# Kernel tuning notes

Hardware: AMD Instinct MI355X
Metric: run time of the kernel (lower is better)

## Reference

```python
import jax, jax.numpy as jnp
import numpy as np

B, T, N_EMBD, HEAD = 8, 2048, 1024, 64


def setup_inputs() -> dict:
    key = jax.random.key(0)
    kx, kq, kk, kv = jax.random.split(key, 4)
    s = 1.0 / np.sqrt(N_EMBD)
    return {
        "x": jax.random.normal(kx, (B, T, N_EMBD), dtype=jnp.float32),
        "Wq": jax.random.normal(kq, (N_EMBD, HEAD), dtype=jnp.float32) * s,
        "Wk": jax.random.normal(kk, (N_EMBD, HEAD), dtype=jnp.float32) * s,
        "Wv": jax.random.normal(kv, (N_EMBD, HEAD), dtype=jnp.float32) * s,
    }


def reference(x, Wq, Wk, Wv):
    # x: [B, T, C] with C = n_embd
    Bs, Ts, C = x.shape
    q = jnp.einsum('btc,ch->bth', x, Wq)  # [B,T,H]
    k = jnp.einsum('btc,ch->bth', x, Wk)
    v = jnp.einsum('btc,ch->bth', x, Wv)
    # NOTE: original scales by C**-0.5 where C = n_embd (input dim), not head_size
    scale = jnp.asarray(C, x.dtype) ** -0.5
    wei = jnp.einsum('bth,bsh->bts', q, k) * scale  # [B,T,T]
    causal = jnp.tril(jnp.ones((Ts, Ts), dtype=bool))
    wei = jnp.where(causal, wei, jnp.asarray(-jnp.inf, wei.dtype))
    wei = jax.nn.softmax(wei, axis=-1)
    out = jnp.einsum('bts,bsh->bth', wei, v)  # [B,T,H]
    return out
```

## Files before the change

kernel.cpp:

```cpp
#include <hip/hip_runtime.h>
#include <hip/hip_bf16.h>
#include <math.h>

#define B_ 8
#define T_ 2048
#define C_ 1024
#define H_ 64

typedef __attribute__((ext_vector_type(8))) __bf16 bf16x8;
typedef __attribute__((ext_vector_type(4))) float f32x4;

static __device__ inline unsigned short f2bf_u(float f) {
    __bf16 b = (__bf16)f;
    return __builtin_bit_cast(unsigned short, b);
}
static __device__ inline unsigned int pack2(float lo, float hi) {
    return (unsigned int)f2bf_u(lo) | ((unsigned int)f2bf_u(hi) << 16);
}

__global__ void prep_w_kernel(const float* __restrict__ Wq,
                              const float* __restrict__ Wk,
                              const float* __restrict__ Wv,
                              unsigned short* __restrict__ Wp) {
    int idx = blockIdx.x * 256 + threadIdx.x;
    if (idx >= C_ * 192) return;
    int k = idx / 192;
    int n = idx % 192;
    const float* W = (n < 64) ? Wq : (n < 128) ? Wk : Wv;
    float val = W[k * 64 + (n & 63)];
    Wp[((size_t)(k >> 5) * 192 + n) * 32 + (k & 31)] = f2bf_u(val);
}

#define XPAD 40
__global__ __launch_bounds__(256, 4) void proj_kernel(
        const float* __restrict__ x, const unsigned short* __restrict__ Wp,
        unsigned short* __restrict__ q, unsigned short* __restrict__ k,
        unsigned short* __restrict__ vT) {
    __shared__ unsigned short xbf[3][16][XPAD];
    const int wave = threadIdx.x >> 6;
    const int lane = threadIdx.x & 63;
    const int col  = lane & 15;
    const int quad = lane >> 4;
    const int row0 = blockIdx.x * 16;
    const int n0   = wave * 48;

    const int srow = lane >> 2;
    const int scol = (lane & 3) * 8;
    const float* sbase = x + (size_t)(row0 + srow) * C_ + scol;

    f32x4 acc[3];
    #pragma unroll
    for (int i = 0; i < 3; i++) acc[i] = (f32x4){0.f, 0.f, 0.f, 0.f};

    if (wave < 2) {
        const float4* p = (const float4*)(sbase + wave * 32);
        float4 u0 = p[0], u1 = p[1];
        bf16x8 w;
        w[0] = (__bf16)u0.x; w[1] = (__bf16)u0.y; w[2] = (__bf16)u0.z; w[3] = (__bf16)u0.w;
        w[4] = (__bf16)u1.x; w[5] = (__bf16)u1.y; w[6] = (__bf16)u1.z; w[7] = (__bf16)u1.w;
        *(bf16x8*)&xbf[wave][srow][scol] = w;
    }
    const unsigned short* wb = Wp + (size_t)(n0 + col) * 32 + quad * 8;
    bf16x8 bcur0 = *(const bf16x8*)(wb);
    bf16x8 bcur1 = *(const bf16x8*)(wb + 16 * 32);
    bf16x8 bcur2 = *(const bf16x8*)(wb + 32 * 32);
    __syncthreads();

    #pragma unroll 2
    for (int kt = 0; kt < 32; kt++) {
        const bool own = (kt + 2 < 32) && (((kt + 2) & 3) == wave);
        float4 u0, u1;
        if (own) {
            const float4* p = (const float4*)(sbase + (kt + 2) * 32);
            u0 = p[0]; u1 = p[1];
        }
        bf16x8 bn0, bn1, bn2;
        if (kt + 1 < 32) {
            const unsigned short* wn = wb + (size_t)(kt + 1) * 192 * 32;
            bn0 = *(const bf16x8*)(wn);
            bn1 = *(const bf16x8*)(wn + 16 * 32);
            bn2 = *(const bf16x8*)(wn + 32 * 32);
        }
        bf16x8 a = *(const bf16x8*)&xbf[kt % 3][col][quad * 8];
        acc[0] = __builtin_amdgcn_mfma_f32_16x16x32_bf16(a, bcur0, acc[0], 0, 0, 0);
        acc[1] = __builtin_amdgcn_mfma_f32_16x16x32_bf16(a, bcur1, acc[1], 0, 0, 0);
        acc[2] = __builtin_amdgcn_mfma_f32_16x16x32_bf16(a, bcur2, acc[2], 0, 0, 0);
        bcur0 = bn0; bcur1 = bn1; bcur2 = bn2;
        if (own) {
            bf16x8 w;
            w[0] = (__bf16)u0.x; w[1] = (__bf16)u0.y; w[2] = (__bf16)u0.z; w[3] = (__bf16)u0.w;
            w[4] = (__bf16)u1.x; w[5] = (__bf16)u1.y; w[6] = (__bf16)u1.z; w[7] = (__bf16)u1.w;
            *(bf16x8*)&xbf[(kt + 2) % 3][srow][scol] = w;
        }
        __syncthreads();
    }

    #pragma unroll
    for (int nt = 0; nt < 3; nt++) {
        f32x4 s = acc[nt];
        int c = n0 + nt * 16;
        int g = c >> 6;
        if (g < 2) {
            unsigned short* dst = (g == 0) ? q : k;
            int cc = (c & 63) + col;
            int grow = row0 + quad * 4;
            #pragma unroll
            for (int r = 0; r < 4; r++)
                dst[(size_t)(grow + r) * 64 + cc] = f2bf_u(s[r]);
        } else {
            int hh = (c - 128) + col;
            int bi = row0 >> 11, trow = (row0 & 2047) + quad * 4;
            ushort4 pk;
            pk.x = f2bf_u(s[0]); pk.y = f2bf_u(s[1]);
            pk.z = f2bf_u(s[2]); pk.w = f2bf_u(s[3]);
            *(ushort4*)(vT + ((size_t)bi * 64 + hh) * T_ + trow) = pk;
        }
    }
}

__global__ __launch_bounds__(256, 4) void attn_kernel(
        const unsigned short* __restrict__ q, const unsigned short* __restrict__ k,
        const unsigned short* __restrict__ vT, float* __restrict__ out) {
    __shared__ unsigned int tbuf[4][2][16 * 20];
    __shared__ float so[4][16][68];
    __shared__ float sl[4][16];
    const int wave = threadIdx.x >> 6;
    const int lane = threadIdx.x & 63;
    const int col  = lane & 15;
    const int quad = lane >> 4;
    const int bi = blockIdx.x & 7;
    const int ti = 127 - (blockIdx.x >> 3);
    const int t0 = ti * 16;
    const unsigned short* qb = q  + (size_t)bi * T_ * 64;
    const unsigned short* kb = k  + (size_t)bi * T_ * 64;
    const unsigned short* vb = vT + (size_t)bi * 64 * T_;

    bf16x8 qf0 = *(const bf16x8*)(qb + (size_t)(t0 + col) * 64 + quad * 8);
    bf16x8 qf1 = *(const bf16x8*)(qb + (size_t)(t0 + col) * 64 + 32 + quad * 8);

    f32x4 o[4];
    #pragma unroll
    for (int i = 0; i < 4; i++) o[i] = (f32x4){0.f, 0.f, 0.f, 0.f};
    float lacc = 0.f;
    const float cs = 0.03125f * 1.44269504088896f;
    const int qrow = t0 + col;

    const int nit = (t0 + 47) >> 5;
    const int ci  = (nit + 3) >> 2;
    const int it0 = wave * ci;
    const int it1 = min(it0 + ci, nit);

    for (int it = it0; it < it1; ++it) {
        const int s0 = it * 32;
        bf16x8 kf00 = *(const bf16x8*)(kb + (size_t)(s0 + col) * 64 + quad * 8);
        bf16x8 kf01 = *(const bf16x8*)(kb + (size_t)(s0 + col) * 64 + 32 + quad * 8);
        bf16x8 kf10 = *(const bf16x8*)(kb + (size_t)(s0 + 16 + col) * 64 + quad * 8);
        bf16x8 kf11 = *(const bf16x8*)(kb + (size_t)(s0 + 16 + col) * 64 + 32 + quad * 8);
        f32x4 sa = (f32x4){0.f, 0.f, 0.f, 0.f};
        f32x4 sb = (f32x4){0.f, 0.f, 0.f, 0.f};
        sa = __builtin_amdgcn_mfma_f32_16x16x32_bf16(kf00, qf0, sa, 0, 0, 0);
        sa = __builtin_amdgcn_mfma_f32_16x16x32_bf16(kf01, qf1, sa, 0, 0, 0);
        sb = __builtin_amdgcn_mfma_f32_16x16x32_bf16(kf10, qf0, sb, 0, 0, 0);
        sb = __builtin_amdgcn_mfma_f32_16x16x32_bf16(kf11, qf1, sb, 0, 0, 0);

        float pa[4], pb[4];
        #pragma unroll
        for (int r = 0; r < 4; r++) {
            int ka = s0 + quad * 4 + r;
            pa[r] = (ka      <= qrow) ? exp2f(sa[r] * cs) : 0.f;
            pb[r] = (ka + 16 <= qrow) ? exp2f(sb[r] * cs) : 0.f;
            lacc += pa[r] + pb[r];
        }
        unsigned int* tb = &tbuf[wave][it & 1][0];
        *(uint2*)&tb[col * 20 + 2 * quad] =
            make_uint2(pack2(pa[0], pa[1]), pack2(pa[2], pa[3]));
        *(uint2*)&tb[col * 20 + 8 + 2 * quad] =
            make_uint2(pack2(pb[0], pb[1]), pack2(pb[2], pb[3]));
        bf16x8 pf = *(const bf16x8*)&tb[col * 20 + 4 * quad];
        #pragma unroll
        for (int ht = 0; ht < 4; ht++) {
            bf16x8 vf = *(const bf16x8*)(vb + (size_t)(ht * 16 + col) * T_ + s0 + quad * 8);
            o[ht] = __builtin_amdgcn_mfma_f32_16x16x32_bf16(vf, pf, o[ht], 0, 0, 0);
        }
    }

    lacc += __shfl_xor(lacc, 16);
    lacc += __shfl_xor(lacc, 32);
    if (quad == 0) sl[wave][col] = lacc;
    #pragma unroll
    for (int ht = 0; ht < 4; ht++)
        *(f32x4*)&so[wave][col][ht * 16 + quad * 4] = o[ht];
    __syncthreads();

    for (int e = threadIdx.x; e < 1024; e += 256) {
        int qq = e >> 6, h = e & 63;
        float L = sl[0][qq] + sl[1][qq] + sl[2][qq] + sl[3][qq];
        float val = so[0][qq][h] + so[1][qq][h] + so[2][qq][h] + so[3][qq][h];
        out[((size_t)bi * T_ + t0 + qq) * 64 + h] = val / L;
    }
}

extern "C" void kernel_launch(void* const* d_in, const int* in_sizes, int n_in,
                              void* d_out, int out_size, void* d_ws, size_t ws_size,
                              hipStream_t stream) {
    const float* x  = (const float*)d_in[0];
    const float* Wq = (const float*)d_in[1];
    const float* Wk = (const float*)d_in[2];
    const float* Wv = (const float*)d_in[3];
    float* out = (float*)d_out;

    unsigned short* Wp  = (unsigned short*)d_ws;
    unsigned short* qws = (unsigned short*)((char*)d_ws + 0x60000);
    unsigned short* kws = (unsigned short*)((char*)d_ws + 0x60000 + 0x200000);
    unsigned short* vws = (unsigned short*)((char*)d_ws + 0x60000 + 0x400000);

    prep_w_kernel<<<(C_ * 192 + 255) / 256, 256, 0, stream>>>(Wq, Wk, Wv, Wp);
    proj_kernel<<<(B_ * T_) / 16, 256, 0, stream>>>(x, Wp, qws, kws, vws);
    attn_kernel<<<(B_ * T_) / 16, 256, 0, stream>>>(qws, kws, vws, out);
}
```

Measured before the change: 161.9 us.

## Stage x in larger double-buffered chunks and split attention keys over eight waves

The projection kernel now has all threads load and convert 256-column chunks of x into a double-buffered shared tile. It syncs once per 8 k-steps instead of every step, prefetching two chunks ahead in registers. The attention kernel moves to 512 threads with eight waves sharing the key range, so each query tile's causal loop is shorter. This costs more shared memory and registers per block, plus a larger final reduction across waves.

```diff
diff --git a/kernel.cpp b/kernel.cpp
--- a/kernel.cpp
+++ b/kernel.cpp
@@ -16,6 +16,12 @@
 }
 static __device__ inline unsigned int pack2(float lo, float hi) {
     return (unsigned int)f2bf_u(lo) | ((unsigned int)f2bf_u(hi) << 16);
+}
+static __device__ inline bf16x8 cvt8(float4 a, float4 b) {
+    bf16x8 w;
+    w[0] = (__bf16)a.x; w[1] = (__bf16)a.y; w[2] = (__bf16)a.z; w[3] = (__bf16)a.w;
+    w[4] = (__bf16)b.x; w[5] = (__bf16)b.y; w[6] = (__bf16)b.z; w[7] = (__bf16)b.w;
+    return w;
 }
 
 __global__ void prep_w_kernel(const float* __restrict__ Wq,
@@ -31,12 +37,12 @@
     Wp[((size_t)(k >> 5) * 192 + n) * 32 + (k & 31)] = f2bf_u(val);
 }
 
-#define XPAD 40
+#define XSTR 264
 __global__ __launch_bounds__(256, 4) void proj_kernel(
         const float* __restrict__ x, const unsigned short* __restrict__ Wp,
         unsigned short* __restrict__ q, unsigned short* __restrict__ k,
         unsigned short* __restrict__ vT) {
-    __shared__ unsigned short xbf[3][16][XPAD];
+    __shared__ unsigned short xb[2][16][XSTR];
     const int wave = threadIdx.x >> 6;
     const int lane = threadIdx.x & 63;
     const int col  = lane & 15;
@@ -44,53 +50,57 @@
     const int row0 = blockIdx.x * 16;
     const int n0   = wave * 48;
 
-    const int srow = lane >> 2;
-    const int scol = (lane & 3) * 8;
-    const float* sbase = x + (size_t)(row0 + srow) * C_ + scol;
+    const int srow = threadIdx.x >> 4;
+    const int sf   = (threadIdx.x & 15) * 16;
+    const float* sb = x + (size_t)(row0 + srow) * C_ + sf;
 
     f32x4 acc[3];
     #pragma unroll
     for (int i = 0; i < 3; i++) acc[i] = (f32x4){0.f, 0.f, 0.f, 0.f};
 
-    if (wave < 2) {
-        const float4* p = (const float4*)(sbase + wave * 32);
-        float4 u0 = p[0], u1 = p[1];
-        bf16x8 w;
-        w[0] = (__bf16)u0.x; w[1] = (__bf16)u0.y; w[2] = (__bf16)u0.z; w[3] = (__bf16)u0.w;
-        w[4] = (__bf16)u1.x; w[5] = (__bf16)u1.y; w[6] = (__bf16)u1.z; w[7] = (__bf16)u1.w;
-        *(bf16x8*)&xbf[wave][srow][scol] = w;
-    }
+    {
+        float4 t0 = *(const float4*)(sb + 0),  t1 = *(const float4*)(sb + 4);
+        float4 t2 = *(const float4*)(sb + 8),  t3 = *(const float4*)(sb + 12);
+        *(bf16x8*)&xb[0][srow][sf]     = cvt8(t0, t1);
+        *(bf16x8*)&xb[0][srow][sf + 8] = cvt8(t2, t3);
+    }
+    float4 l0 = *(const float4*)(sb + 256), l1 = *(const float4*)(sb + 260);
+    float4 l2 = *(const float4*)(sb + 264), l3 = *(const float4*)(sb + 268);
+
     const unsigned short* wb = Wp + (size_t)(n0 + col) * 32 + quad * 8;
     bf16x8 bcur0 = *(const bf16x8*)(wb);
     bf16x8 bcur1 = *(const bf16x8*)(wb + 16 * 32);
     bf16x8 bcur2 = *(const bf16x8*)(wb + 32 * 32);
     __syncthreads();
 
-    #pragma unroll 2
-    for (int kt = 0; kt < 32; kt++) {
-        const bool own = (kt + 2 < 32) && (((kt + 2) & 3) == wave);
-        float4 u0, u1;
-        if (own) {
-            const float4* p = (const float4*)(sbase + (kt + 2) * 32);
-            u0 = p[0]; u1 = p[1];
-        }
-        bf16x8 bn0, bn1, bn2;
-        if (kt + 1 < 32) {
-            const unsigned short* wn = wb + (size_t)(kt + 1) * 192 * 32;
-            bn0 = *(const bf16x8*)(wn);
-            bn1 = *(const bf16x8*)(wn + 16 * 32);
-            bn2 = *(const bf16x8*)(wn + 32 * 32);
-        }
-        bf16x8 a = *(const bf16x8*)&xbf[kt % 3][col][quad * 8];
-        acc[0] = __builtin_amdgcn_mfma_f32_16x16x32_bf16(a, bcur0, acc[0], 0, 0, 0);
-        acc[1] = __builtin_amdgcn_mfma_f32_16x16x32_bf16(a, bcur1, acc[1], 0, 0, 0);
-        acc[2] = __builtin_amdgcn_mfma_f32_16x16x32_bf16(a, bcur2, acc[2], 0, 0, 0);
-        bcur0 = bn0; bcur1 = bn1; bcur2 = bn2;
-        if (own) {
-            bf16x8 w;
-            w[0] = (__bf16)u0.x; w[1] = (__bf16)u0.y; w[2] = (__bf16)u0.z; w[3] = (__bf16)u0.w;
-            w[4] = (__bf16)u1.x; w[5] = (__bf16)u1.y; w[6] = (__bf16)u1.z; w[7] = (__bf16)u1.w;
-            *(bf16x8*)&xbf[(kt + 2) % 3][srow][scol] = w;
+    for (int p = 0; p < 4; ++p) {
+        float4 f0, f1, f2, f3;
+        if (p + 2 < 4) {
+            const float* s2 = sb + (p + 2) * 256;
+            f0 = *(const float4*)(s2 + 0);  f1 = *(const float4*)(s2 + 4);
+            f2 = *(const float4*)(s2 + 8);  f3 = *(const float4*)(s2 + 12);
+        }
+        #pragma unroll
+        for (int kt = 0; kt < 8; ++kt) {
+            const int ktg = p * 8 + kt;
+            bf16x8 bn0, bn1, bn2;
+            if (ktg + 1 < 32) {
+                const unsigned short* wn = wb + (size_t)(ktg + 1) * 192 * 32;
+                bn0 = *(const bf16x8*)(wn);
+                bn1 = *(const bf16x8*)(wn + 16 * 32);
+                bn2 = *(const bf16x8*)(wn + 32 * 32);
+            }
+            bf16x8 a = *(const bf16x8*)&xb[p & 1][col][kt * 32 + quad * 8];
+            acc[0] = __builtin_amdgcn_mfma_f32_16x16x32_bf16(a, bcur0, acc[0], 0, 0, 0);
+            acc[1] = __builtin_amdgcn_mfma_f32_16x16x32_bf16(a, bcur1, acc[1], 0, 0, 0);
+            acc[2] = __builtin_amdgcn_mfma_f32_16x16x32_bf16(a, bcur2, acc[2], 0, 0, 0);
+            bcur0 = bn0; bcur1 = bn1; bcur2 = bn2;
+        }
+        if (p + 1 < 4) {
+            unsigned short* d = &xb[(p + 1) & 1][srow][sf];
+            *(bf16x8*)(d)     = cvt8(l0, l1);
+            *(bf16x8*)(d + 8) = cvt8(l2, l3);
+            l0 = f0; l1 = f1; l2 = f2; l3 = f3;
         }
         __syncthreads();
     }
@@ -118,12 +128,12 @@
     }
 }
 
-__global__ __launch_bounds__(256, 4) void attn_kernel(
+__global__ __launch_bounds__(512, 2) void attn_kernel(
         const unsigned short* __restrict__ q, const unsigned short* __restrict__ k,
         const unsigned short* __restrict__ vT, float* __restrict__ out) {
-    __shared__ unsigned int tbuf[4][2][16 * 20];
-    __shared__ float so[4][16][68];
-    __shared__ float sl[4][16];
+    __shared__ unsigned int tbuf[8][2][16 * 20];
+    __shared__ float so[8][16][68];
+    __shared__ float sl[8][16];
     const int wave = threadIdx.x >> 6;
     const int lane = threadIdx.x & 63;
     const int col  = lane & 15;
@@ -146,7 +156,7 @@
     const int qrow = t0 + col;
 
     const int nit = (t0 + 47) >> 5;
-    const int ci  = (nit + 3) >> 2;
+    const int ci  = (nit + 7) >> 3;
     const int it0 = wave * ci;
     const int it1 = min(it0 + ci, nit);
 
@@ -157,18 +167,18 @@
         bf16x8 kf10 = *(const bf16x8*)(kb + (size_t)(s0 + 16 + col) * 64 + quad * 8);
         bf16x8 kf11 = *(const bf16x8*)(kb + (size_t)(s0 + 16 + col) * 64 + 32 + quad * 8);
         f32x4 sa = (f32x4){0.f, 0.f, 0.f, 0.f};
-        f32x4 sb = (f32x4){0.f, 0.f, 0.f, 0.f};
-        sa = __builtin_amdgcn_mfma_f32_16x16x32_bf16(kf00, qf0, sa, 0, 0, 0);
-        sa = __builtin_amdgcn_mfma_f32_16x16x32_bf16(kf01, qf1, sa, 0, 0, 0);
-        sb = __builtin_amdgcn_mfma_f32_16x16x32_bf16(kf10, qf0, sb, 0, 0, 0);
-        sb = __builtin_amdgcn_mfma_f32_16x16x32_bf16(kf11, qf1, sb, 0, 0, 0);
+        f32x4 sb2 = (f32x4){0.f, 0.f, 0.f, 0.f};
+        sa  = __builtin_amdgcn_mfma_f32_16x16x32_bf16(kf00, qf0, sa, 0, 0, 0);
+        sa  = __builtin_amdgcn_mfma_f32_16x16x32_bf16(kf01, qf1, sa, 0, 0, 0);
+        sb2 = __builtin_amdgcn_mfma_f32_16x16x32_bf16(kf10, qf0, sb2, 0, 0, 0);
+        sb2 = __builtin_amdgcn_mfma_f32_16x16x32_bf16(kf11, qf1, sb2, 0, 0, 0);
 
         float pa[4], pb[4];
         #pragma unroll
         for (int r = 0; r < 4; r++) {
             int ka = s0 + quad * 4 + r;
-            pa[r] = (ka      <= qrow) ? exp2f(sa[r] * cs) : 0.f;
-            pb[r] = (ka + 16 <= qrow) ? exp2f(sb[r] * cs) : 0.f;
+            pa[r] = (ka      <= qrow) ? exp2f(sa[r]  * cs) : 0.f;
+            pb[r] = (ka + 16 <= qrow) ? exp2f(sb2[r] * cs) : 0.f;
             lacc += pa[r] + pb[r];
         }
         unsigned int* tb = &tbuf[wave][it & 1][0];
@@ -192,10 +202,11 @@
         *(f32x4*)&so[wave][col][ht * 16 + quad * 4] = o[ht];
     __syncthreads();
 
-    for (int e = threadIdx.x; e < 1024; e += 256) {
+    for (int e = threadIdx.x; e < 1024; e += 512) {
         int qq = e >> 6, h = e & 63;
-        float L = sl[0][qq] + sl[1][qq] + sl[2][qq] + sl[3][qq];
-        float val = so[0][qq][h] + so[1][qq][h] + so[2][qq][h] + so[3][qq][h];
+        float L = 0.f, val = 0.f;
+        #pragma unroll
+        for (int w = 0; w < 8; w++) { L += sl[w][qq]; val += so[w][qq][h]; }
         out[((size_t)bi * T_ + t0 + qq) * 64 + h] = val / L;
     }
 }
@@ -216,5 +227,5 @@
 
     prep_w_kernel<<<(C_ * 192 + 255) / 256, 256, 0, stream>>>(Wq, Wk, Wv, Wp);
     proj_kernel<<<(B_ * T_) / 16, 256, 0, stream>>>(x, Wp, qws, kws, vws);
-    attn_kernel<<<(B_ * T_) / 16, 256, 0, stream>>>(qws, kws, vws, out);
-}
+    attn_kernel<<<(B_ * T_) / 16, 512, 0, stream>>>(qws, kws, vws, out);
+}
```

Measured after the change: 159.2 us. Within noise of the previous version (-1.7%).
